# Kernel tuning notes

Measured on AMD Instinct MI355X. Metric: run time of the kernel, lower is better.

Reference implementation:

```python
import jax, jax.numpy as jnp
import numpy as np

N, E, M = 100000, 3200000, 1000000  # nodes, message edges, scored move edges
DIN, H = 128, 64


def setup_inputs() -> dict:
    key = jax.random.key(0)
    ks = jax.random.split(key, 20)
    rn = lambda k, shape, s=0.05: (jax.random.normal(k, shape, jnp.float32) * s)
    return {
        "x": jax.random.normal(ks[0], (N, DIN), jnp.float32),
        "edge_index": jax.random.randint(ks[1], (2, E), 0, N, jnp.int64),
        "move_edge_index": jax.random.randint(ks[2], (2, M), 0, N, jnp.int64),
        "lin1_w": rn(ks[3], (DIN, H)), "lin1_b": jnp.zeros((H,), jnp.float32),
        "lin2_w": rn(ks[4], (H, H)), "lin2_b": jnp.zeros((H,), jnp.float32),
        "conv1_wl": rn(ks[5], (H, H)), "conv1_bl": jnp.zeros((H,), jnp.float32),
        "conv1_wr": rn(ks[6], (H, H)),
        "conv2_wl": rn(ks[7], (H, H)), "conv2_bl": jnp.zeros((H,), jnp.float32),
        "conv2_wr": rn(ks[8], (H, H)),
        "mlp_w1": rn(ks[9], (2 * H, H)), "mlp_b1": jnp.zeros((H,), jnp.float32),
        "mlp_w2": rn(ks[10], (H, 1)), "mlp_b2": jnp.zeros((1,), jnp.float32),
    }


def reference(x, edge_index, move_edge_index,
              lin1_w, lin1_b, lin2_w, lin2_b,
              conv1_wl, conv1_bl, conv1_wr,
              conv2_wl, conv2_bl, conv2_wr,
              mlp_w1, mlp_b1, mlp_w2, mlp_b2):
    n = x.shape[0]
    src, dst = edge_index[0], edge_index[1]
    # mean-aggregation degrees (PyG SAGEConv default aggr='mean'; isolated nodes -> 0)
    deg = jax.ops.segment_sum(jnp.ones(src.shape, x.dtype), dst, num_segments=n)
    inv_deg = (jnp.where(deg > 0, 1.0 / jnp.maximum(deg, 1.0), 0.0))[:, None]

    def sage(h, wl, bl, wr):
        # out = W_l @ mean_j h_j + b_l + W_r @ h_i
        agg = jax.ops.segment_sum(h[src], dst, num_segments=n) * inv_deg
        return agg @ wl + bl + h @ wr

    h = jax.nn.relu(x @ lin1_w + lin1_b)
    h = jax.nn.relu(sage(h, conv1_wl, conv1_bl, conv1_wr))
    h = jax.nn.relu(h @ lin2_w + lin2_b)
    h = jax.nn.relu(sage(h, conv2_wl, conv2_bl, conv2_wr))

    # edge scoring: gather src/dst embeddings, concat, 2-layer MLP, tanh
    cat = jnp.concatenate([h[move_edge_index[0]], h[move_edge_index[1]]], axis=1)  # [M, 2H]
    logits = (jax.nn.relu(cat @ mlp_w1 + mlp_b1) @ mlp_w2 + mlp_b2).reshape(-1)
    return jnp.tanh(logits)
```

## Files before the change

### kernel.cpp

```cpp
#include <hip/hip_runtime.h>
#include <math.h>

#define MAXB 512
#define PART_CH 8192
#define PART_BS 1024

typedef _Float16 f16;
typedef __attribute__((ext_vector_type(2))) _Float16 f16x2;
typedef __attribute__((ext_vector_type(4))) _Float16 f16x4;
typedef __attribute__((ext_vector_type(8))) _Float16 f16x8;
typedef __attribute__((ext_vector_type(4))) float f32x4;

static __device__ __forceinline__ unsigned short f2h(float f) {
    f16 h = (f16)f; return *(unsigned short*)&h;
}

__global__ __launch_bounds__(PART_BS) void k_part(const int* __restrict__ src,
                                                  const int* __restrict__ dst,
                                                  int* __restrict__ bcur,
                                                  unsigned* __restrict__ bb,
                                                  int E, int shift, int CAP) {
    __shared__ int h[MAXB], base[MAXB];
    int b0 = blockIdx.x * PART_CH;
    int e1 = min(b0 + PART_CH, E);
    for (int i = threadIdx.x; i < MAXB; i += PART_BS) h[i] = 0;
    __syncthreads();
    for (int i = b0 + threadIdx.x; i < e1; i += PART_BS)
        atomicAdd(&h[dst[i] >> shift], 1);
    __syncthreads();
    for (int i = threadIdx.x; i < MAXB; i += PART_BS) {
        base[i] = h[i] ? atomicAdd(&bcur[i], h[i]) : 0;
        h[i] = 0;
    }
    __syncthreads();
    unsigned mask = (1u << shift) - 1u;
    for (int i = b0 + threadIdx.x; i < e1; i += PART_BS) {
        int d = dst[i];
        int b = d >> shift;
        int r = atomicAdd(&h[b], 1);
        unsigned p = (unsigned)base[b] + (unsigned)r;
        if (p < (unsigned)CAP)
            bb[(size_t)b * CAP + p] = ((unsigned)src[i] << shift) | ((unsigned)d & mask);
    }
}

__global__ __launch_bounds__(512) void k_bfill(const unsigned* __restrict__ bb,
                                               const int* __restrict__ bcur,
                                               int* __restrict__ row_st,
                                               int* __restrict__ row_en,
                                               float* __restrict__ inv_deg,
                                               int* __restrict__ csr,
                                               int N, int shift, int CAP) {
    __shared__ int deg[512], cur[512], s[512];
    int b = blockIdx.x;
    int t = threadIdx.x;
    int lo = b << shift;
    int hi = min(N, (b + 1) << shift);
    int nn = hi - lo;
    unsigned off = (unsigned)b * CAP;
    int cnt = min(bcur[b], CAP);
    unsigned mask = (1u << shift) - 1u;

    deg[t] = 0;
    __syncthreads();
    for (int i = t; i < cnt; i += 512)
        atomicAdd(&deg[bb[off + i] & mask], 1);
    __syncthreads();
    int d = deg[t];
    s[t] = d;
    __syncthreads();
    for (int o = 1; o < 512; o <<= 1) {
        int u = (t >= o) ? s[t - o] : 0;
        __syncthreads();
        s[t] += u;
        __syncthreads();
    }
    int excl = s[t] - d;
    cur[t] = excl;
    if (t < nn) {
        row_st[lo + t] = (int)off + excl;
        row_en[lo + t] = (int)off + excl + d;
        inv_deg[lo + t] = d > 0 ? 1.0f / (float)d : 0.0f;
    }
    __syncthreads();
    for (int i = t; i < cnt; i += 512) {
        unsigned w = bb[off + i];
        int dl = (int)(w & mask);
        int pos = atomicAdd(&cur[dl], 1);
        csr[off + pos] = (int)(w >> shift);
    }
}

__global__ __launch_bounds__(256) void k_prep(
    const float* __restrict__ lin1_w, const float* __restrict__ c1_wl,
    const float* __restrict__ c1_wr, const float* __restrict__ lin2_w,
    const float* __restrict__ c2_wl, const float* __restrict__ c2_wr,
    const float* __restrict__ mlp_w1, const float* __restrict__ mlp_w2,
    unsigned short* __restrict__ Wt) {
    int i = blockIdx.x * 256 + threadIdx.x;
    for (; i < 36928; i += gridDim.x * 256) {
        float v;
        if (i < 8192)       { int j = i;         int n = j >> 7, k = j & 127; v = lin1_w[k * 64 + n]; }
        else if (i < 16384) { int j = i - 8192;  int n = j >> 7, k = j & 127;
                              v = (k < 64) ? c1_wl[k * 64 + n] : c1_wr[(k - 64) * 64 + n]; }
        else if (i < 20480) { int j = i - 16384; int n = j >> 6, k = j & 63;  v = lin2_w[k * 64 + n]; }
        else if (i < 28672) { int j = i - 20480; int n = j >> 7, k = j & 127;
                              v = (k < 64) ? c2_wl[k * 64 + n] : c2_wr[(k - 64) * 64 + n]; }
        else if (i < 32768) { int j = i - 28672; int n = j >> 6, k = j & 63;  v = mlp_w1[k * 64 + n]; }
        else if (i < 36864) { int j = i - 32768; int n = j >> 6, k = j & 63;  v = mlp_w1[(k + 64) * 64 + n]; }
        else                { v = mlp_w2[i - 36864]; }
        Wt[i] = f2h(v);
    }
}

__global__ __launch_bounds__(256) void k_gather_h(
    const _Float16* __restrict__ hh, const int* __restrict__ csr,
    const int* __restrict__ row_st, const int* __restrict__ row_en,
    const float* __restrict__ inv_deg, _Float16* __restrict__ out, int n) {
    int node = (blockIdx.x * 256 + (int)threadIdx.x) >> 6;
    if (node >= n) return;
    int lane = threadIdx.x & 63;
    int g = lane >> 4, sub = lane & 15;
    int base = row_st[node], end = row_en[node];
    float idv = inv_deg[node];
    float a0 = 0.f, a1 = 0.f, a2 = 0.f, a3 = 0.f;
    for (; base < end; base += 32) {
        int last = end - 1;
        int jj[8], sidx[8];
#pragma unroll
        for (int t = 0; t < 8; ++t) {
            jj[t] = base + g + 4 * t;
            sidx[t] = csr[min(jj[t], last)];
        }
        f16x4 u[8];
#pragma unroll
        for (int t = 0; t < 8; ++t)
            u[t] = *(const f16x4*)(hh + (((unsigned)sidx[t] << 6) + ((unsigned)sub << 2)));
#pragma unroll
        for (int t = 0; t < 8; ++t) {
            float m = (jj[t] < end) ? idv : 0.f;
            a0 = fmaf((float)u[t][0], m, a0);
            a1 = fmaf((float)u[t][1], m, a1);
            a2 = fmaf((float)u[t][2], m, a2);
            a3 = fmaf((float)u[t][3], m, a3);
        }
    }
    a0 += __shfl_xor(a0, 16, 64); a1 += __shfl_xor(a1, 16, 64);
    a2 += __shfl_xor(a2, 16, 64); a3 += __shfl_xor(a3, 16, 64);
    a0 += __shfl_xor(a0, 32, 64); a1 += __shfl_xor(a1, 32, 64);
    a2 += __shfl_xor(a2, 32, 64); a3 += __shfl_xor(a3, 32, 64);
    if (g == 0) {
        f16x4 o;
        o[0] = (f16)a0; o[1] = (f16)a1; o[2] = (f16)a2; o[3] = (f16)a3;
        *(f16x4*)(out + (((unsigned)node << 6) + ((unsigned)sub << 2))) = o;
    }
}

__global__ __launch_bounds__(256) void k_mm1(
    const float* __restrict__ x, const unsigned short* __restrict__ Wtg,
    const float* __restrict__ bias, unsigned short* __restrict__ outh, int n) {
    __shared__ alignas(16) unsigned short sW[64 * 136];
    const int tid = threadIdx.x;
    const int row0 = blockIdx.x * 64;
    for (int i = tid; i < 64 * 16; i += 256) {
        int nn = i >> 4, c = i & 15;
        *(uint4*)&sW[(nn * 17 + c) * 8] = *(const uint4*)&Wtg[i * 8];
    }
    __syncthreads();
    const int lane = tid & 63, w = tid >> 6;
    const int m = lane & 15, q = lane >> 4;
    const int gr = min(row0 + 16 * w + m, n - 1);
    const float* ar = x + (size_t)gr * 128;
    f32x4 acc[4];
#pragma unroll
    for (int c = 0; c < 4; ++c) acc[c] = (f32x4){0.f, 0.f, 0.f, 0.f};
#pragma unroll
    for (int kk = 0; kk < 4; ++kk) {
        float4 a0 = *(const float4*)(ar + kk * 32 + q * 8);
        float4 a1 = *(const float4*)(ar + kk * 32 + q * 8 + 4);
        f16x8 af;
        af[0] = (f16)a0.x; af[1] = (f16)a0.y; af[2] = (f16)a0.z; af[3] = (f16)a0.w;
        af[4] = (f16)a1.x; af[5] = (f16)a1.y; af[6] = (f16)a1.z; af[7] = (f16)a1.w;
#pragma unroll
        for (int c = 0; c < 4; ++c) {
            f16x8 bf = *(const f16x8*)&sW[((16 * c + m) * 17 + (kk * 4 + q)) * 8];
            acc[c] = __builtin_amdgcn_mfma_f32_16x16x32_f16(af, bf, acc[c], 0, 0, 0);
        }
    }
#pragma unroll
    for (int c = 0; c < 4; ++c) {
        int col = 16 * c + m;
        float bv = bias[col];
#pragma unroll
        for (int i = 0; i < 4; ++i) {
            int r = row0 + 16 * w + q * 4 + i;
            if (r < n) outh[(size_t)r * 64 + col] = f2h(fmaxf(acc[c][i] + bv, 0.f));
        }
    }
}

__global__ __launch_bounds__(256) void k_mm23(
    const unsigned short* __restrict__ aggH, const unsigned short* __restrict__ h1,
    const unsigned short* __restrict__ Wcg, const float* __restrict__ bl,
    const unsigned short* __restrict__ Wl2g, const float* __restrict__ b2,
    unsigned short* __restrict__ outh, int n) {
    __shared__ alignas(16) unsigned short sm[64 * 72 + 64 * 136];
    unsigned short* hA = sm;
    unsigned short* sW = sm + 64 * 72;
    const int tid = threadIdx.x;
    const int row0 = blockIdx.x * 64;
    for (int i = tid; i < 64 * 16; i += 256) {
        int nn = i >> 4, c = i & 15;
        *(uint4*)&sW[(nn * 17 + c) * 8] = *(const uint4*)&Wcg[i * 8];
    }
    __syncthreads();
    const int lane = tid & 63, w = tid >> 6;
    const int m = lane & 15, q = lane >> 4;
    const int gr = min(row0 + 16 * w + m, n - 1);
    f32x4 acc[4];
#pragma unroll
    for (int c = 0; c < 4; ++c) acc[c] = (f32x4){0.f, 0.f, 0.f, 0.f};
#pragma unroll
    for (int kk = 0; kk < 4; ++kk) {
        const unsigned short* ap = (kk < 2)
            ? (aggH + (size_t)gr * 64 + kk * 32 + q * 8)
            : (h1 + (size_t)gr * 64 + (kk - 2) * 32 + q * 8);
        f16x8 af = *(const f16x8*)ap;
#pragma unroll
        for (int c = 0; c < 4; ++c) {
            f16x8 bf = *(const f16x8*)&sW[((16 * c + m) * 17 + (kk * 4 + q)) * 8];
            acc[c] = __builtin_amdgcn_mfma_f32_16x16x32_f16(af, bf, acc[c], 0, 0, 0);
        }
    }
#pragma unroll
    for (int c = 0; c < 4; ++c) {
        int col = 16 * c + m;
        float bv = bl[col];
#pragma unroll
        for (int i = 0; i < 4; ++i)
            hA[(16 * w + q * 4 + i) * 72 + col] = f2h(fmaxf(acc[c][i] + bv, 0.f));
    }
    __syncthreads();
    for (int i = tid; i < 64 * 8; i += 256) {
        int nn = i >> 3, c = i & 7;
        *(uint4*)&sW[(nn * 9 + c) * 8] = *(const uint4*)&Wl2g[i * 8];
    }
    __syncthreads();
    f32x4 acc2[4];
#pragma unroll
    for (int c = 0; c < 4; ++c) acc2[c] = (f32x4){0.f, 0.f, 0.f, 0.f};
#pragma unroll
    for (int kk = 0; kk < 2; ++kk) {
        f16x8 af = *(const f16x8*)&hA[(16 * w + m) * 72 + kk * 32 + q * 8];
#pragma unroll
        for (int c = 0; c < 4; ++c) {
            f16x8 bf = *(const f16x8*)&sW[((16 * c + m) * 9 + (kk * 4 + q)) * 8];
            acc2[c] = __builtin_amdgcn_mfma_f32_16x16x32_f16(af, bf, acc2[c], 0, 0, 0);
        }
    }
#pragma unroll
    for (int c = 0; c < 4; ++c) {
        int col = 16 * c + m;
        float bv = b2[col];
#pragma unroll
        for (int i = 0; i < 4; ++i) {
            int r = row0 + 16 * w + q * 4 + i;
            if (r < n) outh[(size_t)r * 64 + col] = f2h(fmaxf(acc2[c][i] + bv, 0.f));
        }
    }
}

__global__ __launch_bounds__(256) void k_mm456(
    const unsigned short* __restrict__ aggH, const unsigned short* __restrict__ h3,
    const unsigned short* __restrict__ Wcg, const float* __restrict__ bl,
    const unsigned short* __restrict__ Wpg, const unsigned short* __restrict__ Wqg,
    const float* __restrict__ b1, unsigned short* __restrict__ Ph,
    unsigned short* __restrict__ Qh, int n) {
    __shared__ alignas(16) unsigned short sm[64 * 72 + 2 * 64 * 72];
    unsigned short* hA = sm;
    unsigned short* sW = sm + 64 * 72;
    const int tid = threadIdx.x;
    const int row0 = blockIdx.x * 64;
    for (int i = tid; i < 64 * 16; i += 256) {
        int nn = i >> 4, c = i & 15;
        *(uint4*)&sW[(nn * 17 + c) * 8] = *(const uint4*)&Wcg[i * 8];
    }
    __syncthreads();
    const int lane = tid & 63, w = tid >> 6;
    const int m = lane & 15, q = lane >> 4;
    const int gr = min(row0 + 16 * w + m, n - 1);
    f32x4 acc[4];
#pragma unroll
    for (int c = 0; c < 4; ++c) acc[c] = (f32x4){0.f, 0.f, 0.f, 0.f};
#pragma unroll
    for (int kk = 0; kk < 4; ++kk) {
        const unsigned short* ap = (kk < 2)
            ? (aggH + (size_t)gr * 64 + kk * 32 + q * 8)
            : (h3 + (size_t)gr * 64 + (kk - 2) * 32 + q * 8);
        f16x8 af = *(const f16x8*)ap;
#pragma unroll
        for (int c = 0; c < 4; ++c) {
            f16x8 bf = *(const f16x8*)&sW[((16 * c + m) * 17 + (kk * 4 + q)) * 8];
            acc[c] = __builtin_amdgcn_mfma_f32_16x16x32_f16(af, bf, acc[c], 0, 0, 0);
        }
    }
#pragma unroll
    for (int c = 0; c < 4; ++c) {
        int col = 16 * c + m;
        float bv = bl[col];
#pragma unroll
        for (int i = 0; i < 4; ++i)
            hA[(16 * w + q * 4 + i) * 72 + col] = f2h(fmaxf(acc[c][i] + bv, 0.f));
    }
    __syncthreads();
    for (int i = tid; i < 64 * 8; i += 256) {
        int nn = i >> 3, c = i & 7;
        *(uint4*)&sW[(nn * 9 + c) * 8] = *(const uint4*)&Wpg[i * 8];
        *(uint4*)&sW[4608 + (nn * 9 + c) * 8] = *(const uint4*)&Wqg[i * 8];
    }
    __syncthreads();
    f32x4 accP[4], accQ[4];
#pragma unroll
    for (int c = 0; c < 4; ++c) {
        accP[c] = (f32x4){0.f, 0.f, 0.f, 0.f};
        accQ[c] = (f32x4){0.f, 0.f, 0.f, 0.f};
    }
#pragma unroll
    for (int kk = 0; kk < 2; ++kk) {
        f16x8 af = *(const f16x8*)&hA[(16 * w + m) * 72 + kk * 32 + q * 8];
#pragma unroll
        for (int c = 0; c < 4; ++c) {
            f16x8 bp = *(const f16x8*)&sW[((16 * c + m) * 9 + (kk * 4 + q)) * 8];
            f16x8 bq = *(const f16x8*)&sW[4608 + ((16 * c + m) * 9 + (kk * 4 + q)) * 8];
            accP[c] = __builtin_amdgcn_mfma_f32_16x16x32_f16(af, bp, accP[c], 0, 0, 0);
            accQ[c] = __builtin_amdgcn_mfma_f32_16x16x32_f16(af, bq, accQ[c], 0, 0, 0);
        }
    }
#pragma unroll
    for (int c = 0; c < 4; ++c) {
        int col = 16 * c + m;
        float bv = b1[col];
#pragma unroll
        for (int i = 0; i < 4; ++i) {
            int r = row0 + 16 * w + q * 4 + i;
            if (r < n) {
                Ph[(size_t)r * 64 + col] = f2h(accP[c][i] + bv);
                Qh[(size_t)r * 64 + col] = f2h(accQ[c][i]);
            }
        }
    }
}

__global__ __launch_bounds__(256) void k_score_h(
    const _Float16* __restrict__ P, const _Float16* __restrict__ Q,
    const int* __restrict__ msrc, const int* __restrict__ mdst,
    const _Float16* __restrict__ w2h, const float* __restrict__ b2,
    float* __restrict__ out, int M) {
    int gid = blockIdx.x * 256 + threadIdx.x;
    int e = gid >> 3;
    if (e >= M) return;
    int l = gid & 7;
    int s = msrc[e], d = mdst[e];
    f16x8 p = *(const f16x8*)(P + (((unsigned)s << 6) + ((unsigned)l << 3)));
    f16x8 q = *(const f16x8*)(Q + (((unsigned)d << 6) + ((unsigned)l << 3)));
    f16x8 w = *(const f16x8*)(w2h + ((unsigned)l << 3));
    f16x8 u = p + q;
    f16x8 z = {(f16)0, (f16)0, (f16)0, (f16)0, (f16)0, (f16)0, (f16)0, (f16)0};
    u = __builtin_elementwise_max(u, z);
    float partial;
#if __has_builtin(__builtin_amdgcn_fdot2)
    f16x2 u01 = {u[0], u[1]}, u23 = {u[2], u[3]}, u45 = {u[4], u[5]}, u67 = {u[6], u[7]};
    f16x2 w01 = {w[0], w[1]}, w23 = {w[2], w[3]}, w45 = {w[4], w[5]}, w67 = {w[6], w[7]};
    partial = __builtin_amdgcn_fdot2(u01, w01,
              __builtin_amdgcn_fdot2(u23, w23,
              __builtin_amdgcn_fdot2(u45, w45,
              __builtin_amdgcn_fdot2(u67, w67, 0.f, false), false), false), false);
#else
    partial = 0.f;
#pragma unroll
    for (int i = 0; i < 8; ++i) partial += (float)u[i] * (float)w[i];
#endif
    partial += __shfl_xor(partial, 1, 8);
    partial += __shfl_xor(partial, 2, 8);
    partial += __shfl_xor(partial, 4, 8);
    if (l == 0) {
        float xx = partial + b2[0];
        float t = __expf(2.f * xx);
        out[e] = (t - 1.f) / (t + 1.f);
    }
}

extern "C" void kernel_launch(void* const* d_in, const int* in_sizes, int n_in,
                              void* d_out, int out_size, void* d_ws, size_t ws_size,
                              hipStream_t stream) {
    const float* x      = (const float*)d_in[0];
    const int*   ei     = (const int*)d_in[1];
    const int*   mei    = (const int*)d_in[2];
    const float* lin1_w = (const float*)d_in[3];
    const float* lin1_b = (const float*)d_in[4];
    const float* lin2_w = (const float*)d_in[5];
    const float* lin2_b = (const float*)d_in[6];
    const float* c1_wl  = (const float*)d_in[7];
    const float* c1_bl  = (const float*)d_in[8];
    const float* c1_wr  = (const float*)d_in[9];
    const float* c2_wl  = (const float*)d_in[10];
    const float* c2_bl  = (const float*)d_in[11];
    const float* c2_wr  = (const float*)d_in[12];
    const float* mlp_w1 = (const float*)d_in[13];
    const float* mlp_b1 = (const float*)d_in[14];
    const float* mlp_w2 = (const float*)d_in[15];
    const float* mlp_b2 = (const float*)d_in[16];

    const int N = in_sizes[0] / 128;
    const int E = in_sizes[1] / 2;
    const int M = in_sizes[2] / 2;
    const int* src  = ei;
    const int* dstE = ei + E;
    const int* msrc = mei;
    const int* mdst = mei + M;

    int shift = 8;
    while ((((N - 1) >> shift) + 1) > MAXB) ++shift;
    const int nbuckets = ((N - 1) >> shift) + 1;
    long long avg = (((long long)E << shift) / N) + 1;
    int CAP = (int)((2 * avg + 2047) & ~1023LL);

    const size_t N64 = (size_t)N * 64;
    unsigned short* Hh   = (unsigned short*)d_ws;
    unsigned short* aggH = Hh + N64;
    unsigned short* Qh   = aggH + N64;
    float* inv_deg = (float*)(Qh + N64);
    int*   row_st  = (int*)(inv_deg + N);
    int*   row_en  = row_st + N;
    int*   bcur    = row_en + N;
    unsigned short* Wt = (unsigned short*)(bcur + MAXB);
    int*   csr     = (int*)(Wt + 36928 + 32);
    unsigned* bb   = (unsigned*)Hh;
    float* outf = (float*)d_out;

    const int nbN = (N + 63) / 64;
    const int nbM = (int)(((long long)M * 8 + 255) / 256);
    const int nbG = (int)(((long long)N * 64 + 255) / 256);
    const int nbP = (E + PART_CH - 1) / PART_CH;

    hipMemsetAsync(bcur, 0, MAXB * sizeof(int), stream);
    k_prep<<<64, 256, 0, stream>>>(lin1_w, c1_wl, c1_wr, lin2_w, c2_wl, c2_wr,
                                   mlp_w1, mlp_w2, Wt);
    k_part<<<nbP, PART_BS, 0, stream>>>(src, dstE, bcur, bb, E, shift, CAP);
    k_bfill<<<nbuckets, 512, 0, stream>>>(bb, bcur, row_st, row_en,
                                          inv_deg, csr, N, shift, CAP);

    k_mm1<<<nbN, 256, 0, stream>>>(x, Wt + 0, lin1_b, Hh, N);

    k_gather_h<<<nbG, 256, 0, stream>>>((const _Float16*)Hh, csr, row_st, row_en,
                                        inv_deg, (_Float16*)aggH, N);
    k_mm23<<<nbN, 256, 0, stream>>>(aggH, Hh, Wt + 8192, c1_bl,
                                    Wt + 16384, lin2_b, Hh, N);

    k_gather_h<<<nbG, 256, 0, stream>>>((const _Float16*)Hh, csr, row_st, row_en,
                                        inv_deg, (_Float16*)aggH, N);
    k_mm456<<<nbN, 256, 0, stream>>>(aggH, Hh, Wt + 20480, c2_bl,
                                     Wt + 28672, Wt + 32768, mlp_b1,
                                     Hh, Qh, N);

    k_score_h<<<nbM, 256, 0, stream>>>((const _Float16*)Hh, (const _Float16*)Qh,
                                       msrc, mdst, (const _Float16*)(Wt + 36864),
                                       mlp_b2, outf, M);
}
```

Measured before the change: 379.6 us.

## Pad CSR rows to multiples of 32 with a zero sentinel node to simplify gather

Each node's CSR row is padded to a multiple of 32 entries. The padding slots point to a sentinel node N, whose hidden row is zeroed in k_mm1. This lets the gather kernel load indices with int4 reads and fetch 8 halves per lane without bounds masks. Accumulation uses fdot2 over pairs, and the 1/deg scaling moves to the end. The bcur memset is folded into k_prep to drop one API call. The cost is that padding raises CSR size, and when buckets overflow CAP, edges get truncated.

```diff
diff --git a/kernel.cpp b/kernel.cpp
--- a/kernel.cpp
+++ b/kernel.cpp
@@ -67,7 +67,8 @@
         atomicAdd(&deg[bb[off + i] & mask], 1);
     __syncthreads();
     int d = deg[t];
-    s[t] = d;
+    int pd = (d + 31) & ~31;
+    s[t] = pd;
     __syncthreads();
     for (int o = 1; o < 512; o <<= 1) {
         int u = (t >= o) ? s[t - o] : 0;
@@ -75,19 +76,21 @@
         s[t] += u;
         __syncthreads();
     }
-    int excl = s[t] - d;
+    int excl = min(s[t] - pd, CAP);
+    int pe = min(excl + pd, CAP);
     cur[t] = excl;
     if (t < nn) {
         row_st[lo + t] = (int)off + excl;
-        row_en[lo + t] = (int)off + excl + d;
+        row_en[lo + t] = (int)off + pe;
         inv_deg[lo + t] = d > 0 ? 1.0f / (float)d : 0.0f;
+        for (int j = excl + d; j < pe; ++j) csr[off + j] = N;
     }
     __syncthreads();
     for (int i = t; i < cnt; i += 512) {
         unsigned w = bb[off + i];
         int dl = (int)(w & mask);
         int pos = atomicAdd(&cur[dl], 1);
-        csr[off + pos] = (int)(w >> shift);
+        if (pos < CAP) csr[off + pos] = (int)(w >> shift);
     }
 }
 
@@ -96,7 +99,9 @@
     const float* __restrict__ c1_wr, const float* __restrict__ lin2_w,
     const float* __restrict__ c2_wl, const float* __restrict__ c2_wr,
     const float* __restrict__ mlp_w1, const float* __restrict__ mlp_w2,
-    unsigned short* __restrict__ Wt) {
+    unsigned short* __restrict__ Wt, int* __restrict__ bcur) {
+    if (blockIdx.x == 0)
+        for (int j = threadIdx.x; j < MAXB; j += 256) bcur[j] = 0;
     int i = blockIdx.x * 256 + threadIdx.x;
     for (; i < 36928; i += gridDim.x * 256) {
         float v;
@@ -120,39 +125,46 @@
     int node = (blockIdx.x * 256 + (int)threadIdx.x) >> 6;
     if (node >= n) return;
     int lane = threadIdx.x & 63;
-    int g = lane >> 4, sub = lane & 15;
+    int g = lane >> 3, sub = lane & 7;
     int base = row_st[node], end = row_en[node];
-    float idv = inv_deg[node];
-    float a0 = 0.f, a1 = 0.f, a2 = 0.f, a3 = 0.f;
+    float a[8] = {0.f, 0.f, 0.f, 0.f, 0.f, 0.f, 0.f, 0.f};
+#if __has_builtin(__builtin_amdgcn_fdot2)
+    const f16x2 one2 = {(f16)1.f, (f16)1.f};
+#endif
     for (; base < end; base += 32) {
-        int last = end - 1;
-        int jj[8], sidx[8];
-#pragma unroll
-        for (int t = 0; t < 8; ++t) {
-            jj[t] = base + g + 4 * t;
-            sidx[t] = csr[min(jj[t], last)];
-        }
-        f16x4 u[8];
-#pragma unroll
-        for (int t = 0; t < 8; ++t)
-            u[t] = *(const f16x4*)(hh + (((unsigned)sidx[t] << 6) + ((unsigned)sub << 2)));
-#pragma unroll
-        for (int t = 0; t < 8; ++t) {
-            float m = (jj[t] < end) ? idv : 0.f;
-            a0 = fmaf((float)u[t][0], m, a0);
-            a1 = fmaf((float)u[t][1], m, a1);
-            a2 = fmaf((float)u[t][2], m, a2);
-            a3 = fmaf((float)u[t][3], m, a3);
-        }
-    }
-    a0 += __shfl_xor(a0, 16, 64); a1 += __shfl_xor(a1, 16, 64);
-    a2 += __shfl_xor(a2, 16, 64); a3 += __shfl_xor(a3, 16, 64);
-    a0 += __shfl_xor(a0, 32, 64); a1 += __shfl_xor(a1, 32, 64);
-    a2 += __shfl_xor(a2, 32, 64); a3 += __shfl_xor(a3, 32, 64);
+        int4 s4 = *(const int4*)&csr[base + 4 * g];
+        int sidx[4] = {s4.x, s4.y, s4.z, s4.w};
+        f16x8 u[4];
+#pragma unroll
+        for (int t = 0; t < 4; ++t)
+            u[t] = *(const f16x8*)(hh + (((unsigned)sidx[t] << 6) + ((unsigned)sub << 3)));
+#if __has_builtin(__builtin_amdgcn_fdot2)
+#pragma unroll
+        for (int t = 0; t < 4; t += 2)
+#pragma unroll
+            for (int j = 0; j < 8; ++j) {
+                f16x2 v = {u[t][j], u[t + 1][j]};
+                a[j] = __builtin_amdgcn_fdot2(v, one2, a[j], false);
+            }
+#else
+#pragma unroll
+        for (int t = 0; t < 4; ++t)
+#pragma unroll
+            for (int j = 0; j < 8; ++j) a[j] += (float)u[t][j];
+#endif
+    }
+#pragma unroll
+    for (int j = 0; j < 8; ++j) {
+        a[j] += __shfl_xor(a[j], 8, 64);
+        a[j] += __shfl_xor(a[j], 16, 64);
+        a[j] += __shfl_xor(a[j], 32, 64);
+    }
     if (g == 0) {
-        f16x4 o;
-        o[0] = (f16)a0; o[1] = (f16)a1; o[2] = (f16)a2; o[3] = (f16)a3;
-        *(f16x4*)(out + (((unsigned)node << 6) + ((unsigned)sub << 2))) = o;
+        float idv = inv_deg[node];
+        f16x8 o;
+#pragma unroll
+        for (int j = 0; j < 8; ++j) o[j] = (f16)(a[j] * idv);
+        *(f16x8*)(out + (((unsigned)node << 6) + ((unsigned)sub << 3))) = o;
     }
 }
 
@@ -162,6 +174,8 @@
     __shared__ alignas(16) unsigned short sW[64 * 136];
     const int tid = threadIdx.x;
     const int row0 = blockIdx.x * 64;
+    if (blockIdx.x == 0 && tid < 8)
+        ((uint4*)(outh + (size_t)n * 64))[tid] = (uint4){0, 0, 0, 0};
     for (int i = tid; i < 64 * 16; i += 256) {
         int nn = i >> 4, c = i & 15;
         *(uint4*)&sW[(nn * 17 + c) * 8] = *(const uint4*)&Wtg[i * 8];
@@ -427,7 +441,7 @@
 
     const size_t N64 = (size_t)N * 64;
     unsigned short* Hh   = (unsigned short*)d_ws;
-    unsigned short* aggH = Hh + N64;
+    unsigned short* aggH = Hh + N64 + 64;
     unsigned short* Qh   = aggH + N64;
     float* inv_deg = (float*)(Qh + N64);
     int*   row_st  = (int*)(inv_deg + N);
@@ -443,9 +457,8 @@
     const int nbG = (int)(((long long)N * 64 + 255) / 256);
     const int nbP = (E + PART_CH - 1) / PART_CH;
 
-    hipMemsetAsync(bcur, 0, MAXB * sizeof(int), stream);
     k_prep<<<64, 256, 0, stream>>>(lin1_w, c1_wl, c1_wr, lin2_w, c2_wl, c2_wr,
-                                   mlp_w1, mlp_w2, Wt);
+                                   mlp_w1, mlp_w2, Wt, bcur);
     k_part<<<nbP, PART_BS, 0, stream>>>(src, dstE, bcur, bb, E, shift, CAP);
     k_bfill<<<nbuckets, 512, 0, stream>>>(bb, bcur, row_st, row_en,
                                           inv_deg, csr, N, shift, CAP);
```

New measurement: 389.3 us. 2.5% more time.
